# Performance work log

Hardware: AMD Instinct MI355X
Metric: run time of the kernel (lower is better)

## Reference

```python
import jax, jax.numpy as jnp
import numpy as np

N = 50000   # nodes
E = 800000  # edges (avg degree 16)
D = 128     # feature dim
H = 4       # heads
DH = D // H # head dim


def setup_inputs() -> dict:
    key = jax.random.key(0)
    ks = jax.random.split(key, 12)
    s = 1.0 / np.sqrt(D)
    return {
        "x": jax.random.normal(ks[0], (N, D), dtype=jnp.float32),
        "src": jax.random.randint(ks[1], (E,), 0, N, dtype=jnp.int32),
        "dst": jax.random.randint(ks[2], (E,), 0, N, dtype=jnp.int32),
        # input_linear: Linear(d, d)
        "W_in": jax.random.uniform(ks[3], (D, D), jnp.float32, -s, s),
        "b_in": jax.random.uniform(ks[4], (D,), jnp.float32, -s, s),
        # attn_linear_u: Linear(d, n_heads), attn_linear_v: Linear(d, n_heads, bias=False)
        "W_au": jax.random.uniform(ks[5], (D, H), jnp.float32, -s, s),
        "b_au": jax.random.uniform(ks[6], (H,), jnp.float32, -s, s),
        "W_av": jax.random.uniform(ks[7], (D, H), jnp.float32, -s, s),
        # FFN: Linear(d, d) -> ReLU -> Linear(d, d)  (dropout=0)
        "W_f1": jax.random.uniform(ks[8], (D, D), jnp.float32, -s, s),
        "b_f1": jax.random.uniform(ks[9], (D,), jnp.float32, -s, s),
        "W_f2": jax.random.uniform(ks[10], (D, D), jnp.float32, -s, s),
        "b_f2": jax.random.uniform(ks[11], (D,), jnp.float32, -s, s),
    }


def reference(x, src, dst, W_in, b_in, W_au, b_au, W_av, W_f1, b_f1, W_f2, b_f2):
    h = x @ W_in + b_in                                # [N, D]
    su = h @ W_au + b_au                               # [N, H]
    sv = h @ W_av                                      # [N, H]
    # u_add_v gather + LeakyReLU
    e = jax.nn.leaky_relu(su[src] + sv[dst], 0.2)      # [E, H]
    # edge_softmax: softmax over incoming edges of each dst node
    m = jax.ops.segment_max(e, dst, num_segments=N)    # [N, H]
    ex = jnp.exp(e - m[dst])                           # [E, H]
    z = jax.ops.segment_sum(ex, dst, num_segments=N)   # [N, H]
    p = ex / z[dst]                                    # [E, H]
    # u_mul_e_sum: weighted aggregation (note reshape order (N, d_head, H))
    hu = h.reshape(N, DH, H)[src]                      # [E, DH, H]
    agg = jax.ops.segment_sum(hu * p[:, None, :], dst, num_segments=N)  # [N, DH, H]
    y = agg.reshape(N, D)
    # FFN
    return jax.nn.relu(y @ W_f1 + b_f1) @ W_f2 + b_f2
```

## Files before the change

kernel.cpp:

```cpp
#include <hip/hip_runtime.h>
#include <hip/hip_bf16.h>
#include <math.h>

#define D 128
#define NHEADS 4

static constexpr int CAP  = 64;
static constexpr int CSTR = 16;

typedef __attribute__((ext_vector_type(8))) short bf16x8;
typedef __attribute__((ext_vector_type(4))) float f32x4;

__device__ __forceinline__ float4 ld4(const float* p) {
    return *reinterpret_cast<const float4*>(p);
}
__device__ __forceinline__ float4 fma4(float a, float4 b, float4 c) {
    c.x = fmaf(a, b.x, c.x); c.y = fmaf(a, b.y, c.y);
    c.z = fmaf(a, b.z, c.z); c.w = fmaf(a, b.w, c.w);
    return c;
}
__device__ __forceinline__ unsigned short f2bf(float f) {
    __hip_bfloat16 b = __float2bfloat16(f);
    return __builtin_bit_cast(unsigned short, b);
}
__device__ __forceinline__ float bf2f(unsigned short u) {
    return __uint_as_float((unsigned)u << 16);
}
__device__ __forceinline__ void cvt_hilo(const float4& a0, const float4& a1,
                                         bf16x8& hi, bf16x8& lo) {
    float v[8] = {a0.x, a0.y, a0.z, a0.w, a1.x, a1.y, a1.z, a1.w};
#pragma unroll
    for (int i = 0; i < 8; ++i) {
        unsigned short h = f2bf(v[i]);
        hi[i] = (short)h;
        lo[i] = (short)f2bf(v[i] - bf2f(h));
    }
}

template<int MODE>
__global__ __launch_bounds__(256)
void mfma_gemm128(const float* __restrict__ A, const float* __restrict__ W,
                  const float* __restrict__ bias, float* __restrict__ out,
                  unsigned short* __restrict__ out16, int N, int ntiles,
                  const float* __restrict__ Wau, const float* __restrict__ bau,
                  const float* __restrict__ Wav,
                  float* __restrict__ su, float* __restrict__ sv)
{
    __shared__ unsigned short wh[D * D];
    __shared__ unsigned short wl[D * D];

    const int t = threadIdx.x;
#pragma unroll
    for (int i = 0; i < 16; ++i) {
        int g = t + i * 256;
        int col = g & 127;
        int k0 = (g >> 7) << 2;
        short4 h4, l4;
#pragma unroll
        for (int k = 0; k < 4; ++k) {
            float v = W[(size_t)(k0 + k) * D + col];
            unsigned short hb = f2bf(v);
            ((short*)&h4)[k] = (short)hb;
            ((short*)&l4)[k] = (short)f2bf(v - bf2f(hb));
        }
        int off = col * D + (k0 ^ ((col & 7) << 3));
        *reinterpret_cast<short4*>(&wh[off]) = h4;
        *reinterpret_cast<short4*>(&wl[off]) = l4;
    }
    __syncthreads();

    const int wid  = t >> 6;
    const int lane = t & 63;
    const int q8   = (lane >> 4) * 8;

    float4 bau4 = {0, 0, 0, 0};
    if constexpr (MODE == 0) bau4 = ld4(bau);

    for (int tile = blockIdx.x; tile < ntiles; tile += gridDim.x) {
        const int rbase = tile * 64 + wid * 16;
        const int arow  = rbase + (lane & 15);

        bf16x8 ahi[4], alo[4];
#pragma unroll
        for (int ks = 0; ks < 4; ++ks) {
            float4 a0 = {0, 0, 0, 0}, a1 = {0, 0, 0, 0};
            if (arow < N) {
                const float* ap = A + (size_t)arow * D + 32 * ks + q8;
                a0 = ld4(ap); a1 = ld4(ap + 4);
            }
            cvt_hilo(a0, a1, ahi[ks], alo[ks]);
        }

        f32x4 acc[8];
#pragma unroll
        for (int ct = 0; ct < 8; ++ct) acc[ct] = (f32x4){0.f, 0.f, 0.f, 0.f};

#pragma unroll
        for (int ct = 0; ct < 8; ++ct) {
            const int colb = ct * 16 + (lane & 15);
            const int sw   = (colb & 7) << 3;
            bf16x8 bh[4], bl[4];
#pragma unroll
            for (int ks = 0; ks < 4; ++ks) {
                int off = colb * D + ((32 * ks + q8) ^ sw);
                bh[ks] = *reinterpret_cast<const bf16x8*>(&wh[off]);
                bl[ks] = *reinterpret_cast<const bf16x8*>(&wl[off]);
            }
#pragma unroll
            for (int ks = 0; ks < 4; ++ks) {
                acc[ct] = __builtin_amdgcn_mfma_f32_16x16x32_bf16(ahi[ks], bh[ks], acc[ct], 0, 0, 0);
                acc[ct] = __builtin_amdgcn_mfma_f32_16x16x32_bf16(alo[ks], bh[ks], acc[ct], 0, 0, 0);
                acc[ct] = __builtin_amdgcn_mfma_f32_16x16x32_bf16(ahi[ks], bl[ks], acc[ct], 0, 0, 0);
            }
        }

        const int crow0 = rbase + (lane >> 4) * 4;

        float4 s_u[4], s_v[4];
        if constexpr (MODE == 0) {
#pragma unroll
            for (int j = 0; j < 4; ++j) { s_u[j] = {0,0,0,0}; s_v[j] = {0,0,0,0}; }
        }

#pragma unroll
        for (int ct = 0; ct < 8; ++ct) {
            const int col = ct * 16 + (lane & 15);
            const float bv = bias[col];
            float4 wau4, wav4;
            if constexpr (MODE == 0) {
                wau4 = ld4(Wau + col * NHEADS);
                wav4 = ld4(Wav + col * NHEADS);
            }
#pragma unroll
            for (int j = 0; j < 4; ++j) {
                const int r = crow0 + j;
                float v = acc[ct][j] + bv;
                if constexpr (MODE == 1) v = fmaxf(v, 0.f);
                if (r < N) {
                    if constexpr (MODE == 0)
                        out16[(size_t)r * D + col] = f2bf(v);
                    else
                        out[(size_t)r * D + col] = v;
                }
                if constexpr (MODE == 0) {
                    s_u[j] = fma4(v, wau4, s_u[j]);
                    s_v[j] = fma4(v, wav4, s_v[j]);
                }
            }
        }

        if constexpr (MODE == 0) {
#pragma unroll
            for (int j = 0; j < 4; ++j) {
#pragma unroll
                for (int d2 = 1; d2 < 16; d2 <<= 1) {
                    s_u[j].x += __shfl_xor(s_u[j].x, d2); s_u[j].y += __shfl_xor(s_u[j].y, d2);
                    s_u[j].z += __shfl_xor(s_u[j].z, d2); s_u[j].w += __shfl_xor(s_u[j].w, d2);
                    s_v[j].x += __shfl_xor(s_v[j].x, d2); s_v[j].y += __shfl_xor(s_v[j].y, d2);
                    s_v[j].z += __shfl_xor(s_v[j].z, d2); s_v[j].w += __shfl_xor(s_v[j].w, d2);
                }
            }
            if ((lane & 15) == 0) {
#pragma unroll
                for (int j = 0; j < 4; ++j) {
                    const int r = crow0 + j;
                    if (r < N) {
                        float4 u = s_u[j];
                        u.x += bau4.x; u.y += bau4.y; u.z += bau4.z; u.w += bau4.w;
                        *reinterpret_cast<float4*>(su + (size_t)r * NHEADS) = u;
                        *reinterpret_cast<float4*>(sv + (size_t)r * NHEADS) = s_v[j];
                    }
                }
            }
        }
    }
}

__global__ __launch_bounds__(256)
void scatter_kernel(const int* __restrict__ src, const int* __restrict__ dst,
                    int* __restrict__ cursor, unsigned short* __restrict__ slot, int E) {
    const int i0 = (blockIdx.x * 256 + threadIdx.x) * 4;
    if (i0 + 4 <= E) {
        int4 d4 = *reinterpret_cast<const int4*>(dst + i0);
        int4 s4 = *reinterpret_cast<const int4*>(src + i0);
        int p0 = atomicAdd(&cursor[d4.x * CSTR], 1);
        int p1 = atomicAdd(&cursor[d4.y * CSTR], 1);
        int p2 = atomicAdd(&cursor[d4.z * CSTR], 1);
        int p3 = atomicAdd(&cursor[d4.w * CSTR], 1);
        if (p0 < CAP) slot[((size_t)d4.x << 6) + p0] = (unsigned short)s4.x;
        if (p1 < CAP) slot[((size_t)d4.y << 6) + p1] = (unsigned short)s4.y;
        if (p2 < CAP) slot[((size_t)d4.z << 6) + p2] = (unsigned short)s4.z;
        if (p3 < CAP) slot[((size_t)d4.w << 6) + p3] = (unsigned short)s4.w;
    } else {
        for (int i = i0; i < E; ++i) {
            int d = dst[i];
            int p = atomicAdd(&cursor[d * CSTR], 1);
            if (p < CAP) slot[((size_t)d << 6) + p] = (unsigned short)src[i];
        }
    }
}

__global__ __launch_bounds__(256)
void agg_kernel(const unsigned short* __restrict__ h16, const float* __restrict__ su,
                const float* __restrict__ sv, const int* __restrict__ cursor,
                const unsigned short* __restrict__ slot, float* __restrict__ y, int N)
{
    __shared__ int   s_s[4][64];
    __shared__ float s_p[4][64][4];

    const int wslot = threadIdx.x >> 6;
    const int lane  = threadIdx.x & 63;
    const int n = blockIdx.x * 4 + wslot;
    if (n >= N) return;

    const int deg = min(cursor[n * CSTR], CAP);

    if (deg == 0) {
        *reinterpret_cast<float2*>(y + (size_t)n * D + lane * 2) = float2{0.f, 0.f};
        return;
    }

    const float4 sv4 = ld4(sv + (size_t)n * NHEADS);

    float4 z4 = {0.f, 0.f, 0.f, 0.f};
    float2 acc = {0.f, 0.f};
    const int psel = (lane & 1) * 2;

    int sj = 0;
    float4 ex4 = {0.f, 0.f, 0.f, 0.f};
    if (lane < deg) {
        sj = slot[((size_t)n << 6) + lane];
        float4 u = ld4(su + (size_t)sj * NHEADS);
        float e0 = u.x + sv4.x, e1 = u.y + sv4.y, e2 = u.z + sv4.z, e3 = u.w + sv4.w;
        e0 = e0 >= 0.f ? e0 : 0.2f * e0; e1 = e1 >= 0.f ? e1 : 0.2f * e1;
        e2 = e2 >= 0.f ? e2 : 0.2f * e2; e3 = e3 >= 0.f ? e3 : 0.2f * e3;
        ex4.x = __expf(e0); ex4.y = __expf(e1);
        ex4.z = __expf(e2); ex4.w = __expf(e3);
    }
    float4 tt = ex4;
#pragma unroll
    for (int d2 = 1; d2 < 64; d2 <<= 1) {
        tt.x += __shfl_xor(tt.x, d2); tt.y += __shfl_xor(tt.y, d2);
        tt.z += __shfl_xor(tt.z, d2); tt.w += __shfl_xor(tt.w, d2);
    }
    z4.x += tt.x; z4.y += tt.y; z4.z += tt.z; z4.w += tt.w;

    s_s[wslot][lane] = sj;
    *reinterpret_cast<float4*>(&s_p[wslot][lane][0]) = ex4;
    __builtin_amdgcn_wave_barrier();

#pragma unroll 4
    for (int j = 0; j < deg; ++j) {
        int s = s_s[wslot][j];
        float2 p2 = *reinterpret_cast<const float2*>(&s_p[wslot][j][psel]);
        unsigned u = *reinterpret_cast<const unsigned*>(h16 + ((size_t)s << 7) + (lane << 1));
        acc.x = fmaf(p2.x, __uint_as_float(u << 16), acc.x);
        acc.y = fmaf(p2.y, __uint_as_float(u & 0xffff0000u), acc.y);
    }

    const float2 z2 = (lane & 1) ? float2{z4.z, z4.w} : float2{z4.x, z4.y};
    float2 o;
    o.x = acc.x / z2.x;
    o.y = acc.y / z2.y;
    *reinterpret_cast<float2*>(y + (size_t)n * D + lane * 2) = o;
}

extern "C" void kernel_launch(void* const* d_in, const int* in_sizes, int n_in,
                              void* d_out, int out_size, void* d_ws, size_t ws_size,
                              hipStream_t stream) {
    const float* x    = (const float*)d_in[0];
    const int*   src  = (const int*)d_in[1];
    const int*   dst  = (const int*)d_in[2];
    const float* W_in = (const float*)d_in[3];
    const float* b_in = (const float*)d_in[4];
    const float* W_au = (const float*)d_in[5];
    const float* b_au = (const float*)d_in[6];
    const float* W_av = (const float*)d_in[7];
    const float* W_f1 = (const float*)d_in[8];
    const float* b_f1 = (const float*)d_in[9];
    const float* W_f2 = (const float*)d_in[10];
    const float* b_f2 = (const float*)d_in[11];
    float* out = (float*)d_out;

    const int N = in_sizes[0] / D;
    const int E = in_sizes[1];

    char* ws = (char*)d_ws;
    size_t o = 0;
    auto alloc = [&](size_t bytes) -> void* {
        void* p = ws + o;
        o += (bytes + 255) & ~(size_t)255;
        return p;
    };
    void*           bufA   = alloc((size_t)N * D * 4);
    float*          y      = (float*)alloc((size_t)N * D * 4);
    float*          su     = (float*)alloc((size_t)N * NHEADS * 4);
    float*          sv     = (float*)alloc((size_t)N * NHEADS * 4);
    int*            cursor = (int*)alloc((size_t)N * CSTR * 4);
    unsigned short* slot   = (unsigned short*)alloc((size_t)N * CAP * 2);

    unsigned short* h16 = (unsigned short*)bufA;
    float*          hid = (float*)bufA;

    hipMemsetAsync(cursor, 0, (size_t)N * CSTR * 4, stream);

    const int ntiles = (N + 63) / 64;
    const int ggrid  = (ntiles + 1) / 2;
    const int sgrid  = (E + 1023) / 1024;

    scatter_kernel<<<sgrid, 256, 0, stream>>>(src, dst, cursor, slot, E);

    mfma_gemm128<0><<<ggrid, 256, 0, stream>>>(x, W_in, b_in, nullptr, h16, N, ntiles,
                                               W_au, b_au, W_av, su, sv);

    agg_kernel<<<(N + 3) / 4, 256, 0, stream>>>(h16, su, sv, cursor, slot, y, N);

    mfma_gemm128<1><<<ggrid, 256, 0, stream>>>(y, W_f1, b_f1, hid, nullptr, N, ntiles,
                                               nullptr, nullptr, nullptr, nullptr, nullptr);
    mfma_gemm128<2><<<ggrid, 256, 0, stream>>>(hid, W_f2, b_f2, out, nullptr, N, ntiles,
                                               nullptr, nullptr, nullptr, nullptr, nullptr);
}
```

Before: 158.1 us.

## Replace global-atomic edge scatter with two-pass bucketed binning via shared memory

Swaps the per-edge global atomicAdd scatter into padded per-node cursors for a two-stage counting sort. A bin kernel histograms edges into 256-node buckets in shared memory and appends packed (src, local dst) words to bucket buffers. A csr kernel then loads each bucket into LDS and fills per-node slot lists with shared atomics, also writing a compact degree array. The goal is to cut heavy global atomic traffic and the large memset, at the cost of an extra kernel launch, an intermediate buffer, and a fixed bucket capacity that silently drops edges if it overflows.

```diff
diff --git a/kernel.cpp b/kernel.cpp
--- a/kernel.cpp
+++ b/kernel.cpp
@@ -6,7 +6,8 @@
 #define NHEADS 4
 
 static constexpr int CAP  = 64;
-static constexpr int CSTR = 16;
+static constexpr int CAPB = 5120;
+static constexpr int EB   = 4096;
 
 typedef __attribute__((ext_vector_type(8))) short bf16x8;
 typedef __attribute__((ext_vector_type(4))) float f32x4;
@@ -177,32 +178,71 @@
 }
 
 __global__ __launch_bounds__(256)
-void scatter_kernel(const int* __restrict__ src, const int* __restrict__ dst,
-                    int* __restrict__ cursor, unsigned short* __restrict__ slot, int E) {
-    const int i0 = (blockIdx.x * 256 + threadIdx.x) * 4;
-    if (i0 + 4 <= E) {
-        int4 d4 = *reinterpret_cast<const int4*>(dst + i0);
-        int4 s4 = *reinterpret_cast<const int4*>(src + i0);
-        int p0 = atomicAdd(&cursor[d4.x * CSTR], 1);
-        int p1 = atomicAdd(&cursor[d4.y * CSTR], 1);
-        int p2 = atomicAdd(&cursor[d4.z * CSTR], 1);
-        int p3 = atomicAdd(&cursor[d4.w * CSTR], 1);
-        if (p0 < CAP) slot[((size_t)d4.x << 6) + p0] = (unsigned short)s4.x;
-        if (p1 < CAP) slot[((size_t)d4.y << 6) + p1] = (unsigned short)s4.y;
-        if (p2 < CAP) slot[((size_t)d4.z << 6) + p2] = (unsigned short)s4.z;
-        if (p3 < CAP) slot[((size_t)d4.w << 6) + p3] = (unsigned short)s4.w;
-    } else {
-        for (int i = i0; i < E; ++i) {
-            int d = dst[i];
-            int p = atomicAdd(&cursor[d * CSTR], 1);
-            if (p < CAP) slot[((size_t)d << 6) + p] = (unsigned short)src[i];
-        }
-    }
+void bin_kernel(const int* __restrict__ src, const int* __restrict__ dst,
+                int* __restrict__ bucket_cnt ,
+                unsigned* __restrict__ bucket_buf, int E, int NB)
+{
+    __shared__ int hist[256];
+    __shared__ int base[256];
+    __shared__ int off[256];
+    const int t = threadIdx.x;
+    hist[t] = 0; off[t] = 0;
+    __syncthreads();
+
+    const int e0 = blockIdx.x * EB;
+#pragma unroll
+    for (int j = 0; j < EB / 256; ++j) {
+        int idx = e0 + j * 256 + t;
+        if (idx < E) atomicAdd(&hist[dst[idx] >> 8], 1);
+    }
+    __syncthreads();
+    if (t < NB) {
+        int hv = hist[t];
+        base[t] = hv ? atomicAdd(&bucket_cnt[t * 16], hv) : 0;
+    }
+    __syncthreads();
+#pragma unroll
+    for (int j = 0; j < EB / 256; ++j) {
+        int idx = e0 + j * 256 + t;
+        if (idx < E) {
+            int d = dst[idx];
+            int b = d >> 8;
+            int p = base[b] + atomicAdd(&off[b], 1);
+            if (p < CAPB)
+                bucket_buf[(size_t)b * CAPB + p] =
+                    (unsigned)(src[idx] | ((d & 255) << 16));
+        }
+    }
+}
+
+__global__ __launch_bounds__(256)
+void csr_kernel(const int* __restrict__ bucket_cnt, const unsigned* __restrict__ bucket_buf,
+                unsigned short* __restrict__ slot, int* __restrict__ deg, int N)
+{
+    __shared__ unsigned ebuf[CAPB];
+    __shared__ int cur[256];
+    const int b = blockIdx.x;
+    const int t = threadIdx.x;
+    const int cnt = min(bucket_cnt[b * 16], CAPB);
+    cur[t] = 0;
+    for (int i = t; i < cnt; i += 256)
+        ebuf[i] = bucket_buf[(size_t)b * CAPB + i];
+    __syncthreads();
+    for (int i = t; i < cnt; i += 256) {
+        unsigned e = ebuf[i];
+        int dl = e >> 16;
+        int pos = atomicAdd(&cur[dl], 1);
+        if (pos < CAP)
+            slot[(((size_t)(b * 256 + dl)) << 6) + pos] = (unsigned short)(e & 0xffff);
+    }
+    __syncthreads();
+    int n = b * 256 + t;
+    if (n < N) deg[n] = min(cur[t], CAP);
 }
 
 __global__ __launch_bounds__(256)
 void agg_kernel(const unsigned short* __restrict__ h16, const float* __restrict__ su,
-                const float* __restrict__ sv, const int* __restrict__ cursor,
+                const float* __restrict__ sv, const int* __restrict__ deg_arr,
                 const unsigned short* __restrict__ slot, float* __restrict__ y, int N)
 {
     __shared__ int   s_s[4][64];
@@ -213,7 +253,7 @@
     const int n = blockIdx.x * 4 + wslot;
     if (n >= N) return;
 
-    const int deg = min(cursor[n * CSTR], CAP);
+    const int deg = deg_arr[n];
 
     if (deg == 0) {
         *reinterpret_cast<float2*>(y + (size_t)n * D + lane * 2) = float2{0.f, 0.f};
@@ -284,6 +324,7 @@
 
     const int N = in_sizes[0] / D;
     const int E = in_sizes[1];
+    const int NB = (N + 255) / 256;
 
     char* ws = (char*)d_ws;
     size_t o = 0;
@@ -292,28 +333,32 @@
         o += (bytes + 255) & ~(size_t)255;
         return p;
     };
-    void*           bufA   = alloc((size_t)N * D * 4);
-    float*          y      = (float*)alloc((size_t)N * D * 4);
-    float*          su     = (float*)alloc((size_t)N * NHEADS * 4);
-    float*          sv     = (float*)alloc((size_t)N * NHEADS * 4);
-    int*            cursor = (int*)alloc((size_t)N * CSTR * 4);
-    unsigned short* slot   = (unsigned short*)alloc((size_t)N * CAP * 2);
+    void*           bufA       = alloc((size_t)N * D * 4);
+    float*          y          = (float*)alloc((size_t)N * D * 4);
+    float*          su         = (float*)alloc((size_t)N * NHEADS * 4);
+    float*          sv         = (float*)alloc((size_t)N * NHEADS * 4);
+    int*            bucket_cnt = (int*)alloc((size_t)NB * 16 * 4);
+    unsigned*       bucket_buf = (unsigned*)alloc((size_t)NB * CAPB * 4);
+    unsigned short* slot       = (unsigned short*)alloc((size_t)NB * 256 * CAP * 2);
+    int*            deg        = (int*)alloc((size_t)N * 4);
 
     unsigned short* h16 = (unsigned short*)bufA;
     float*          hid = (float*)bufA;
 
-    hipMemsetAsync(cursor, 0, (size_t)N * CSTR * 4, stream);
+    hipMemsetAsync(bucket_cnt, 0, (size_t)NB * 16 * 4, stream);
 
     const int ntiles = (N + 63) / 64;
     const int ggrid  = (ntiles + 1) / 2;
-    const int sgrid  = (E + 1023) / 1024;
-
-    scatter_kernel<<<sgrid, 256, 0, stream>>>(src, dst, cursor, slot, E);
+    const int bgrid  = (E + EB - 1) / EB;
+
+    bin_kernel<<<bgrid, 256, 0, stream>>>(src, dst, bucket_cnt, bucket_buf, E, NB);
 
     mfma_gemm128<0><<<ggrid, 256, 0, stream>>>(x, W_in, b_in, nullptr, h16, N, ntiles,
                                                W_au, b_au, W_av, su, sv);
 
-    agg_kernel<<<(N + 3) / 4, 256, 0, stream>>>(h16, su, sv, cursor, slot, y, N);
+    csr_kernel<<<NB, 256, 0, stream>>>(bucket_cnt, bucket_buf, slot, deg, N);
+
+    agg_kernel<<<(N + 3) / 4, 256, 0, stream>>>(h16, su, sv, deg, slot, y, N);
 
     mfma_gemm128<1><<<ggrid, 256, 0, stream>>>(y, W_f1, b_f1, hid, nullptr, N, ntiles,
                                                nullptr, nullptr, nullptr, nullptr, nullptr);
```

Measured after the change: 134.8 us. 14.7% less time.
